# Kernel tuning notes

Hardware: AMD Instinct MI355X
Metric: run time of the kernel (lower is better)

The kernel has to match this reference:

```python
import jax, jax.numpy as jnp
import numpy as np

# --- static configuration (matches init_kwargs / input_specs) ---
N = 256            # n_channels
M_MODES = 8        # n_modes
S = 64             # n_subjects
VEC = N * (N + 1) // 2
EPSILON = 1e-6     # epsilon added to covariance diagonal
DIAG_SHIFT = 1e-5  # TFP FillScaleTriL default diag_shift

# --- TFP fill_triangular index maps (computed once with numpy) ---
# fill_triangular: vec -> tril matrix via concat([x[n:], reverse(x)]).reshape(n,n)
_x = np.arange(VEC)
_idx_mat = np.concatenate([_x[N:], _x[::-1]]).reshape(N, N)
_ROWS, _COLS = np.tril_indices(N)
_PERM = _idx_mat[_ROWS, _COLS]            # vec index feeding each tril slot
_INV = np.empty(VEC, dtype=np.int64)      # tril-slot index for each vec position
_INV[_PERM] = np.arange(VEC)
_DIAG = np.arange(N)


def _softplus_inverse(x):
    # log(expm1(x)), numerically stable
    return x + jnp.log(-jnp.expm1(-x))


def _fill_scale_tril_inverse(cov):
    """cov (..., N, N) SPD -> unconstrained vec (..., VEC). Matches
    Chain([CholeskyOuterProduct, FillScaleTriL]).inverse with default diag bijector."""
    L = jnp.linalg.cholesky(cov)                       # CholeskyOuterProduct.inverse
    d = _softplus_inverse(L[..., _DIAG, _DIAG] - DIAG_SHIFT)
    L = L.at[..., _DIAG, _DIAG].set(d)
    vals = L[..., _ROWS, _COLS]                        # (..., VEC) in tril order
    return vals[..., _INV]                             # reorder to TFP vec order


def _fill_scale_tril_forward(vec):
    """vec (..., VEC) -> SPD cov (..., N, N). Matches bijector forward."""
    L = jnp.zeros(vec.shape[:-1] + (N, N), dtype=vec.dtype)
    L = L.at[..., _ROWS, _COLS].set(vec[..., _PERM])
    d = jax.nn.softplus(L[..., _DIAG, _DIAG]) + DIAG_SHIFT
    L = L.at[..., _DIAG, _DIAG].set(d)
    return jnp.einsum('...ij,...kj->...ik', L, L)      # CholeskyOuterProduct


def setup_inputs() -> dict:
    key = jax.random.key(0)
    k1, k2 = jax.random.split(key)
    A = 0.1 * jax.random.normal(k1, (M_MODES, N, N), dtype=jnp.float32)
    group_map = jnp.einsum('mij,mkj->mik', A, A) + jnp.eye(N, dtype=jnp.float32)
    dev = 0.05 * jax.random.normal(k2, (S, M_MODES, VEC), dtype=jnp.float32)
    return {"group_map": group_map, "dev": dev}


def reference(group_map, dev):
    # which_map == 'covariances'
    flat = _fill_scale_tril_inverse(group_map)         # (M, VEC)
    subject_flat = flat[None, :, :] + dev              # (S, M, VEC)
    subject_map = _fill_scale_tril_forward(subject_flat)  # (S, M, N, N)
    # add_epsilon(..., diag=True)
    eye = jnp.eye(N, dtype=subject_map.dtype)
    return subject_map + jnp.float32(EPSILON) * eye
```

## Files before the change

kernel.cpp:

```cpp
#include <hip/hip_runtime.h>
#include <hip/hip_bf16.h>

#define NCH 256
#define VEC 32896

typedef __attribute__((ext_vector_type(4)))  float f32x4;
typedef __attribute__((ext_vector_type(8)))  short short8;
typedef __attribute__((ext_vector_type(32))) float f32x32;
typedef __attribute__((ext_vector_type(4)))  unsigned short u16x4;
typedef __attribute__((ext_vector_type(4), aligned(4))) float f32x4u;

template <int C>
__device__ __forceinline__ f32x32& sel(f32x32& a, f32x32& b, f32x32& c, f32x32& d) {
    if constexpr (C == 0) return a;
    else if constexpr (C == 1) return b;
    else if constexpr (C == 2) return c;
    else return d;
}

__device__ __forceinline__ void load_chunk(f32x32& V, const float* src) {
#pragma unroll
    for (int k = 0; k < 32; k += 4) {
        const float4 q = *reinterpret_cast<const float4*>(src + k);
        V[k] = q.x; V[k + 1] = q.y; V[k + 2] = q.z; V[k + 3] = q.w;
    }
}

template <int C, int P>
__device__ __forceinline__ void trail(f32x32& V, const f32x32& Lr,
                                      const float (&Ap)[256][34], int h, int band) {
    const int gc = 2 * C + h;
    if (gc >= P + 1 && gc <= 2 * band + 1) {
#pragma unroll
        for (int k = 0; k < 32; ++k) {
            float acc = V[k];
            const float* rowp = Ap[gc * 32 + k];
#pragma unroll
            for (int q = 0; q < 32; q += 2) {
                const float2 pv = *reinterpret_cast<const float2*>(rowp + q);
                acc = fmaf(-Lr[q],     pv.x, acc);
                acc = fmaf(-Lr[q + 1], pv.y, acc);
            }
            V[k] = acc;
        }
    }
}

template <int P>
__device__ __forceinline__ void panel_step(
        float* __restrict__ tv, float (&Ap)[256][34], float (&Dblk)[32][34],
        float (&Dinv)[32], f32x32& v0, f32x32& v1, f32x32& v2, f32x32& v3,
        int t, int lane, int h, int band, int i) {
    constexpr int ho = P & 1, lc = P >> 1, pbase = P << 5;

    if (h == ho && (i >> 5) == P) {
        const int r = i & 31;
        f32x32& V = sel<lc>(v0, v1, v2, v3);
#pragma unroll
        for (int k = 0; k < 32; ++k) Dblk[r][k] = V[k];
    }
    __syncthreads();

    if (t < 64) {
        const int r = lane & 31;
        f32x32 a;
#pragma unroll
        for (int k = 0; k < 32; ++k) a[k] = Dblk[r][k];
        float mydiag = 1.0f;
#pragma unroll
        for (int j = 0; j < 32; ++j) {
            const float dj  = __shfl(a[j], j);
            const float d   = sqrtf(dj);
            const float inv = 1.0f / d;
            const float lrj = a[j] * inv;
            a[j] = (r == j) ? d : lrj;
            if (r == j) mydiag = d;
#pragma unroll
            for (int k = j + 1; k < 32; ++k) {
                const float lkj = __shfl(a[j], k);
                a[k] = fmaf(-a[j], lkj, a[k]);
            }
        }
        if (lane < 32) {
            const int gr = pbase + r;
            const int tb = gr * (gr + 1) / 2 + pbase;
#pragma unroll
            for (int k = 0; k < 32; ++k) {
                Dblk[r][k] = a[k];
                if (k < r) tv[tb + k] = a[k];
            }
            Dinv[r] = 1.0f / mydiag;
            const float x = mydiag - 1e-5f;
            tv[tb + r] = x + logf(-expm1f(-x));
        }
    }
    __syncthreads();

    const bool below = (i >= pbase + 32);
    if (h == ho && below) {
        f32x32& V = sel<lc>(v0, v1, v2, v3);
#pragma unroll
        for (int k = 0; k < 32; ++k) {
            float xk = V[k];
#pragma unroll
            for (int q = 0; q < k; ++q) xk = fmaf(-V[q], Dblk[k][q], xk);
            V[k] = xk * Dinv[k];
        }
        const int tb = i * (i + 1) / 2 + pbase;
#pragma unroll
        for (int k = 0; k < 32; ++k) { Ap[i][k] = V[k]; tv[tb + k] = V[k]; }
    }
    __syncthreads();

    if (below) {
        f32x32 Lr;
        if (h == ho) {
            Lr = sel<lc>(v0, v1, v2, v3);
        } else {
#pragma unroll
            for (int k = 0; k < 32; ++k) Lr[k] = Ap[i][k];
        }
        trail<0, P>(v0, Lr, Ap, h, band);
        trail<1, P>(v1, Lr, Ap, h, band);
        trail<2, P>(v2, Lr, Ap, h, band);
        trail<3, P>(v3, Lr, Ap, h, band);
    }
    __syncthreads();
}

__global__ void __launch_bounds__(512)
__attribute__((amdgpu_waves_per_eu(2, 2)))
chol_kernel(const float* __restrict__ G, float* __restrict__ t_out) {
    const int t    = threadIdx.x;
    const int w    = t >> 6;
    const int lane = t & 63;
    const int band = (0x4B >> (2 * (w >> 1))) & 3;
    const int h    = (0xA5 >> w) & 1;
    const int i    = band * 64 + lane;

    const float* A  = G + (size_t)blockIdx.x * NCH * NCH;
    float*       tv = t_out + (size_t)blockIdx.x * VEC;

    __shared__ float Ap[256][34];
    __shared__ float Dblk[32][34];
    __shared__ float Dinv[32];

    f32x32 v0, v1, v2, v3;
    {
        const float* base = A + (size_t)i * NCH + h * 32;
        load_chunk(v0, base);
        load_chunk(v1, base + 64);
        load_chunk(v2, base + 128);
        load_chunk(v3, base + 192);
    }

    panel_step<0>(tv, Ap, Dblk, Dinv, v0, v1, v2, v3, t, lane, h, band, i);
    panel_step<1>(tv, Ap, Dblk, Dinv, v0, v1, v2, v3, t, lane, h, band, i);
    panel_step<2>(tv, Ap, Dblk, Dinv, v0, v1, v2, v3, t, lane, h, band, i);
    panel_step<3>(tv, Ap, Dblk, Dinv, v0, v1, v2, v3, t, lane, h, band, i);
    panel_step<4>(tv, Ap, Dblk, Dinv, v0, v1, v2, v3, t, lane, h, band, i);
    panel_step<5>(tv, Ap, Dblk, Dinv, v0, v1, v2, v3, t, lane, h, band, i);
    panel_step<6>(tv, Ap, Dblk, Dinv, v0, v1, v2, v3, t, lane, h, band, i);
    panel_step<7>(tv, Ap, Dblk, Dinv, v0, v1, v2, v3, t, lane, h, band, i);
}

__global__ __launch_bounds__(1024)
void syrk_kernel(const float* __restrict__ dev, const float* __restrict__ t_in,
                 float* __restrict__ out) {
    extern __shared__ char smem[];
    const int bid  = blockIdx.x;
    const int m    = bid & 7;
    const int tid  = threadIdx.x;
    const int lane = tid & 63;
    const int w    = tid >> 6;

    const float* dv = dev  + (size_t)bid * VEC;
    const float* tv = t_in + (size_t)m * VEC;
    float* C = out + (size_t)bid * NCH * NCH;

#pragma unroll 4
    for (int it = 0; it < 16; ++it) {
        const int pos = it * 4096 + tid * 4;
        const int r  = pos >> 8;
        const int c0 = pos & 255;
        u16x4 ov = {0, 0, 0, 0};
        if (c0 <= r) {
            float4 dvv;
            if (r < 128) {
                dvv = *reinterpret_cast<const float4*>(dv + pos + 256);
            } else {
                const float4 t4 = *reinterpret_cast<const float4*>(dv + (65532 - pos));
                dvv.x = t4.w; dvv.y = t4.z; dvv.z = t4.y; dvv.w = t4.x;
            }
            const int s0 = r * (r + 1) / 2 + c0;
            const f32x4u tvv = *reinterpret_cast<const f32x4u*>(tv + s0);
            const float dva[4] = {dvv.x, dvv.y, dvv.z, dvv.w};
#pragma unroll
            for (int j = 0; j < 4; ++j) {
                const int c = c0 + j;
                if (c <= r) {
                    float u = tvv[j] + dva[j];
                    if (c == r) {
                        u = (u > 20.0f) ? u : log1pf(expf(u));
                        u += 1e-5f;
                    }
                    __hip_bfloat16 hb = __float2bfloat16(u);
                    ov[j] = *reinterpret_cast<unsigned short*>(&hb);
                }
            }
        }
        int byte = (r << 9) + (c0 << 1);
        byte ^= (r & 7) << 4;
        *reinterpret_cast<u16x4*>(smem + byte) = ov;
    }
    __syncthreads();

    const int I    = w;
    const int lrow = lane & 15;
    const int kq   = lane >> 4;
    const int nkmax = (I + 2) >> 1;
    const int arow  = I * 16 + lrow;

    short8 a0 = {0,0,0,0,0,0,0,0}, a1 = a0, a2 = a0, a3 = a0,
           a4 = a0, a5 = a0, a6 = a0, a7 = a0;
#define LOADA(K, AV) if (K < nkmax) { \
        int ab = (arow << 9) + ((K * 32 + kq * 8) << 1); ab ^= (arow & 7) << 4; \
        AV = *reinterpret_cast<const short8*>(smem + ab); }
    LOADA(0, a0) LOADA(1, a1) LOADA(2, a2) LOADA(3, a3)
    LOADA(4, a4) LOADA(5, a5) LOADA(6, a6) LOADA(7, a7)
#undef LOADA

    for (int J = 0; J < 16; ++J) {
        const int nk = ((I < J ? I : J) + 2) >> 1;
        f32x4 acc = {0.f, 0.f, 0.f, 0.f};
        const int brow = J * 16 + lrow;
#define STEP(K, AV) if (K < nk) { \
        int bb = (brow << 9) + ((K * 32 + kq * 8) << 1); bb ^= (brow & 7) << 4; \
        const short8 b = *reinterpret_cast<const short8*>(smem + bb); \
        acc = __builtin_amdgcn_mfma_f32_16x16x32_bf16(AV, b, acc, 0, 0, 0); }
        STEP(0, a0) STEP(1, a1) STEP(2, a2) STEP(3, a3)
        STEP(4, a4) STEP(5, a5) STEP(6, a6) STEP(7, a7)
#undef STEP
        const int crow = I * 16 + kq * 4;
        const int ccol = J * 16 + lrow;
#pragma unroll
        for (int q = 0; q < 4; ++q) {
            float vv = acc[q];
            if (crow + q == ccol) vv += 1e-6f;
            C[(crow + q) * NCH + ccol] = vv;
        }
    }
}

extern "C" void kernel_launch(void* const* d_in, const int* in_sizes, int n_in,
                              void* d_out, int out_size, void* d_ws, size_t ws_size,
                              hipStream_t stream) {
    const float* group_map = (const float*)d_in[0];
    const float* dev       = (const float*)d_in[1];
    float* out  = (float*)d_out;
    float* t_ws = (float*)d_ws;

    (void)in_sizes; (void)n_in; (void)out_size; (void)ws_size;

    (void)hipFuncSetAttribute((const void*)syrk_kernel,
                              hipFuncAttributeMaxDynamicSharedMemorySize, 131072);

    chol_kernel<<<8, 512, 0, stream>>>(group_map, t_ws);
    syrk_kernel<<<512, 1024, 131072, stream>>>(dev, t_ws, out);
}
```

Measured before the change: 452.7 us.

## Split Cholesky row ownership across 16 waves with two column chunks each

```diff
diff --git a/kernel.cpp b/kernel.cpp
--- a/kernel.cpp
+++ b/kernel.cpp
@@ -11,11 +11,8 @@
 typedef __attribute__((ext_vector_type(4), aligned(4))) float f32x4u;
 
 template <int C>
-__device__ __forceinline__ f32x32& sel(f32x32& a, f32x32& b, f32x32& c, f32x32& d) {
-    if constexpr (C == 0) return a;
-    else if constexpr (C == 1) return b;
-    else if constexpr (C == 2) return c;
-    else return d;
+__device__ __forceinline__ f32x32& sel2(f32x32& a, f32x32& b) {
+    if constexpr (C == 0) return a; else return b;
 }
 
 __device__ __forceinline__ void load_chunk(f32x32& V, const float* src) {
@@ -26,22 +23,25 @@
     }
 }
 
-template <int C, int P>
-__device__ __forceinline__ void trail(f32x32& V, const f32x32& Lr,
-                                      const float (&Ap)[256][34], int h, int band) {
-    const int gc = 2 * C + h;
+template <int IDX, int P>
+__device__ __forceinline__ void trail2(f32x32& V, const f32x32& Lr,
+                                       const float (&Ap)[256][34],
+                                       int q, int band, bool below) {
+    const int gc = (IDX == 0) ? q : q + 4;
     if (gc >= P + 1 && gc <= 2 * band + 1) {
-#pragma unroll
-        for (int k = 0; k < 32; ++k) {
-            float acc = V[k];
-            const float* rowp = Ap[gc * 32 + k];
-#pragma unroll
-            for (int q = 0; q < 32; q += 2) {
-                const float2 pv = *reinterpret_cast<const float2*>(rowp + q);
-                acc = fmaf(-Lr[q],     pv.x, acc);
-                acc = fmaf(-Lr[q + 1], pv.y, acc);
-            }
-            V[k] = acc;
+        if (below) {
+#pragma unroll
+            for (int k = 0; k < 32; ++k) {
+                float acc = V[k];
+                const float* rowp = Ap[gc * 32 + k];
+#pragma unroll
+                for (int u = 0; u < 32; u += 2) {
+                    const float2 pv = *reinterpret_cast<const float2*>(rowp + u);
+                    acc = fmaf(-Lr[u],     pv.x, acc);
+                    acc = fmaf(-Lr[u + 1], pv.y, acc);
+                }
+                V[k] = acc;
+            }
         }
     }
 }
@@ -49,13 +49,13 @@
 template <int P>
 __device__ __forceinline__ void panel_step(
         float* __restrict__ tv, float (&Ap)[256][34], float (&Dblk)[32][34],
-        float (&Dinv)[32], f32x32& v0, f32x32& v1, f32x32& v2, f32x32& v3,
-        int t, int lane, int h, int band, int i) {
-    constexpr int ho = P & 1, lc = P >> 1, pbase = P << 5;
-
-    if (h == ho && (i >> 5) == P) {
+        float (&Dinv)[32], f32x32& v0, f32x32& v1,
+        int t, int lane, int q, int band, int i) {
+    constexpr int qo = P & 3, lc = P >> 2, pbase = P << 5;
+
+    if (q == qo && (i >> 5) == P) {
         const int r = i & 31;
-        f32x32& V = sel<lc>(v0, v1, v2, v3);
+        f32x32& V = sel2<lc>(v0, v1);
 #pragma unroll
         for (int k = 0; k < 32; ++k) Dblk[r][k] = V[k];
     }
@@ -97,13 +97,13 @@
     __syncthreads();
 
     const bool below = (i >= pbase + 32);
-    if (h == ho && below) {
-        f32x32& V = sel<lc>(v0, v1, v2, v3);
+    if (q == qo && below) {
+        f32x32& V = sel2<lc>(v0, v1);
 #pragma unroll
         for (int k = 0; k < 32; ++k) {
             float xk = V[k];
 #pragma unroll
-            for (int q = 0; q < k; ++q) xk = fmaf(-V[q], Dblk[k][q], xk);
+            for (int u = 0; u < k; ++u) xk = fmaf(-V[u], Dblk[k][u], xk);
             V[k] = xk * Dinv[k];
         }
         const int tb = i * (i + 1) / 2 + pbase;
@@ -112,30 +112,29 @@
     }
     __syncthreads();
 
-    if (below) {
+    {
         f32x32 Lr;
-        if (h == ho) {
-            Lr = sel<lc>(v0, v1, v2, v3);
-        } else {
-#pragma unroll
-            for (int k = 0; k < 32; ++k) Lr[k] = Ap[i][k];
-        }
-        trail<0, P>(v0, Lr, Ap, h, band);
-        trail<1, P>(v1, Lr, Ap, h, band);
-        trail<2, P>(v2, Lr, Ap, h, band);
-        trail<3, P>(v3, Lr, Ap, h, band);
-    }
-    __syncthreads();
-}
-
-__global__ void __launch_bounds__(512)
-__attribute__((amdgpu_waves_per_eu(2, 2)))
+        if (below) {
+            if (q == qo) {
+                Lr = sel2<lc>(v0, v1);
+            } else {
+#pragma unroll
+                for (int k = 0; k < 32; ++k) Lr[k] = Ap[i][k];
+            }
+        }
+        trail2<0, P>(v0, Lr, Ap, q, band, below);
+        trail2<1, P>(v1, Lr, Ap, q, band, below);
+    }
+    __syncthreads();
+}
+
+__global__ void __launch_bounds__(1024)
 chol_kernel(const float* __restrict__ G, float* __restrict__ t_out) {
     const int t    = threadIdx.x;
     const int w    = t >> 6;
     const int lane = t & 63;
-    const int band = (0x4B >> (2 * (w >> 1))) & 3;
-    const int h    = (0xA5 >> w) & 1;
+    const int q    = w >> 2;
+    const int band = (w & 3) ^ (w >> 2);
     const int i    = band * 64 + lane;
 
     const float* A  = G + (size_t)blockIdx.x * NCH * NCH;
@@ -145,23 +144,21 @@
     __shared__ float Dblk[32][34];
     __shared__ float Dinv[32];
 
-    f32x32 v0, v1, v2, v3;
+    f32x32 v0, v1;
     {
-        const float* base = A + (size_t)i * NCH + h * 32;
+        const float* base = A + (size_t)i * NCH + q * 32;
         load_chunk(v0, base);
-        load_chunk(v1, base + 64);
-        load_chunk(v2, base + 128);
-        load_chunk(v3, base + 192);
-    }
-
-    panel_step<0>(tv, Ap, Dblk, Dinv, v0, v1, v2, v3, t, lane, h, band, i);
-    panel_step<1>(tv, Ap, Dblk, Dinv, v0, v1, v2, v3, t, lane, h, band, i);
-    panel_step<2>(tv, Ap, Dblk, Dinv, v0, v1, v2, v3, t, lane, h, band, i);
-    panel_step<3>(tv, Ap, Dblk, Dinv, v0, v1, v2, v3, t, lane, h, band, i);
-    panel_step<4>(tv, Ap, Dblk, Dinv, v0, v1, v2, v3, t, lane, h, band, i);
-    panel_step<5>(tv, Ap, Dblk, Dinv, v0, v1, v2, v3, t, lane, h, band, i);
-    panel_step<6>(tv, Ap, Dblk, Dinv, v0, v1, v2, v3, t, lane, h, band, i);
-    panel_step<7>(tv, Ap, Dblk, Dinv, v0, v1, v2, v3, t, lane, h, band, i);
+        load_chunk(v1, base + 128);
+    }
+
+    panel_step<0>(tv, Ap, Dblk, Dinv, v0, v1, t, lane, q, band, i);
+    panel_step<1>(tv, Ap, Dblk, Dinv, v0, v1, t, lane, q, band, i);
+    panel_step<2>(tv, Ap, Dblk, Dinv, v0, v1, t, lane, q, band, i);
+    panel_step<3>(tv, Ap, Dblk, Dinv, v0, v1, t, lane, q, band, i);
+    panel_step<4>(tv, Ap, Dblk, Dinv, v0, v1, t, lane, q, band, i);
+    panel_step<5>(tv, Ap, Dblk, Dinv, v0, v1, t, lane, q, band, i);
+    panel_step<6>(tv, Ap, Dblk, Dinv, v0, v1, t, lane, q, band, i);
+    panel_step<7>(tv, Ap, Dblk, Dinv, v0, v1, t, lane, q, band, i);
 }
 
 __global__ __launch_bounds__(1024)
@@ -265,6 +262,6 @@
     (void)hipFuncSetAttribute((const void*)syrk_kernel,
                               hipFuncAttributeMaxDynamicSharedMemorySize, 131072);
 
-    chol_kernel<<<8, 512, 0, stream>>>(group_map, t_ws);
+    chol_kernel<<<8, 1024, 0, stream>>>(group_map, t_ws);
     syrk_kernel<<<512, 1024, 131072, stream>>>(dev, t_ws, out);
 }
```

Measured after the change: 969.3 us. 114% more time.
